# Kernel optimization log

Measured on AMD Instinct MI355X. Metric: run time of the kernel, lower is better.

The kernel has to match this reference:

```python
import jax, jax.numpy as jnp
import numpy as np

DIM = 256
N_STATE = 8
DT_RANK = 16  # ceil(dim/16)
D_CONV = 4
HIDDEN = 128  # dim * rank_ratio
EPS = 1e-6


def rmsnorm(x, w):
    # matches torch: x / (||x||_2 / sqrt(d) + eps) * w
    norm = jnp.sqrt(jnp.sum(x * x, axis=-1, keepdims=True))
    return x / (norm / np.sqrt(x.shape[-1]) + EPS) * w


def dwconv1d(x, w, b, pad_l, pad_r):
    # x: (b, l, c); w: (c, 1, k) depthwise
    out = jax.lax.conv_general_dilated(
        x.transpose(0, 2, 1), w, window_strides=(1,),
        padding=[(pad_l, pad_r)], dimension_numbers=('NCH', 'OIH', 'NCH'),
        feature_group_count=w.shape[0])
    return (out + b[None, :, None]).transpose(0, 2, 1)


def selective_scan(x, delta, A, Bm, Cm, D):
    # x, delta: (b,l,d); A: (d,n); Bm, Cm: (b,l,n); D: (d,)
    dA = jnp.exp(delta[..., None] * A)                     # (b,l,d,n)
    dBx = (delta * x)[..., None] * Bm[:, :, None, :]       # (b,l,d,n)

    def step(h, inp):
        dA_t, dBx_t, C_t = inp
        h = dA_t * h + dBx_t                               # (b,d,n)
        y = jnp.einsum('bdn,bn->bd', h, C_t)
        return h, y

    h0 = jnp.zeros((x.shape[0],) + A.shape, dtype=x.dtype)
    _, ys = jax.lax.scan(step, h0,
                         (dA.transpose(1, 0, 2, 3), dBx.transpose(1, 0, 2, 3),
                          Cm.transpose(1, 0, 2)))
    return ys.transpose(1, 0, 2) + x * D                   # (b,l,d)


def mamba_branch(x, ctx, conv_w, conv_b, xproj_w, dtproj_w, dtproj_b, A_log, D):
    xc = jax.nn.silu(dwconv1d(x, conv_w, conv_b, D_CONV - 1, 0))  # causal conv
    x_dbl = ctx @ xproj_w.T                                  # (b,l,r+2n)
    dt, Bm, Cm = jnp.split(x_dbl, [DT_RANK, DT_RANK + N_STATE], axis=-1)
    delta = jax.nn.softplus(dt @ dtproj_w.T + dtproj_b)
    A = -jnp.exp(A_log)
    return selective_scan(xc, delta, A, Bm, Cm, D)


def setup_inputs() -> dict:
    key = jax.random.key(0)
    ks = jax.random.split(key, 24)
    B, L, D = 4, 64 * 64, DIM
    s = 0.02
    A_log_init = jnp.log(jnp.broadcast_to(jnp.arange(1, N_STATE + 1, dtype=jnp.float32), (D, N_STATE)))
    dt_bias = jnp.full((D,), jnp.log(jnp.expm1(0.01)), dtype=jnp.float32)
    inp = {
        'x0': jax.random.normal(ks[0], (B, L, D), jnp.float32),
        'x1': jax.random.normal(ks[1], (B, L, D), jnp.float32),
        'w_norm0': jnp.ones((D,), jnp.float32),
        'w_norm1': jnp.ones((D,), jnp.float32),
        'in_proj_w': jax.random.normal(ks[2], (2 * D, D), jnp.float32) * s,
        'conv_w_f': jax.random.normal(ks[3], (D, 1, D_CONV), jnp.float32) * 0.3,
        'conv_b_f': jnp.zeros((D,), jnp.float32),
        'xproj_w_f': jax.random.normal(ks[4], (DT_RANK + 2 * N_STATE, D), jnp.float32) * s,
        'dtproj_w_f': jax.random.normal(ks[5], (D, DT_RANK), jnp.float32) * 0.1,
        'dtproj_b_f': dt_bias,
        'A_log_f': A_log_init,
        'D_f': jnp.ones((D,), jnp.float32),
        'conv_w_bw': jax.random.normal(ks[6], (D, 1, D_CONV), jnp.float32) * 0.3,
        'conv_b_bw': jnp.zeros((D,), jnp.float32),
        'xproj_w_bw': jax.random.normal(ks[7], (DT_RANK + 2 * N_STATE, D), jnp.float32) * s,
        'dtproj_w_bw': jax.random.normal(ks[8], (D, DT_RANK), jnp.float32) * 0.1,
        'dtproj_b_bw': dt_bias,
        'A_log_bw': A_log_init,
        'D_bw': jnp.ones((D,), jnp.float32),
        'norm_y_w': jnp.ones((D,), jnp.float32),
        'out_proj_w': jax.random.normal(ks[9], (D, D), jnp.float32) * s,
        'fc1_w': jax.random.normal(ks[10], (HIDDEN, D), jnp.float32) * s,
        'dw_w': jax.random.normal(ks[11], (HIDDEN, 1, 3), jnp.float32) * 0.3,
        'dw_b': jnp.zeros((HIDDEN,), jnp.float32),
        'fc2_w': jax.random.normal(ks[12], (D, HIDDEN), jnp.float32) * s,
    }
    return inp


def reference(x0, x1, w_norm0, w_norm1, in_proj_w, conv_w_f, conv_b_f, xproj_w_f,
              dtproj_w_f, dtproj_b_f, A_log_f, D_f, conv_w_bw, conv_b_bw,
              xproj_w_bw, dtproj_w_bw, dtproj_b_bw, A_log_bw, D_bw, norm_y_w,
              out_proj_w, fc1_w, dw_w, dw_b, fc2_w):
    residual = x0
    h0 = rmsnorm(x0, w_norm0)
    h1 = rmsnorm(x1, w_norm1)
    # cross-Mamba: main stream x0 -> x,z; extra_emb x1 -> dt/B/C
    xz = h0 @ in_proj_w.T
    xin, z = jnp.split(xz, 2, axis=-1)
    y_f = mamba_branch(xin, h1, conv_w_f, conv_b_f, xproj_w_f, dtproj_w_f,
                       dtproj_b_f, A_log_f, D_f)
    y_b = jnp.flip(mamba_branch(jnp.flip(xin, 1), jnp.flip(h1, 1), conv_w_bw,
                                conv_b_bw, xproj_w_bw, dtproj_w_bw, dtproj_b_bw,
                                A_log_bw, D_bw), 1)
    y = (y_f + y_b) * 0.5          # if_devide_out=True (bidirectional)
    y = rmsnorm(y, norm_y_w)       # use_norm=True
    y = y * jax.nn.silu(z)
    x = y @ out_proj_w.T + residual
    # LowRankFeedForward (dropout = identity at eval)
    m = x @ fc1_w.T
    m = jax.nn.silu(dwconv1d(m, dw_w, dw_b, 1, 1))
    m = m @ fc2_w.T
    return x + m
```

## Files before the change

kernel.cpp:

```cpp
#include <hip/hip_runtime.h>
#include <math.h>
#include <cstddef>

#define BB 4
#define LL 4096
#define DD 256
#define NST 8
#define RANK 16
#define HID 128
#define BL (BB*LL)
#define BLD ((size_t)BL*DD)
#define CH 256
#define CLEN 16
#define XZS 512

typedef __bf16 bf16x8 __attribute__((ext_vector_type(8)));
typedef float  f32x4  __attribute__((ext_vector_type(4)));

__device__ __forceinline__ float siluf(float x){ return x / (1.f + __expf(-x)); }
__device__ __forceinline__ float softplus_fast(float x){
  float r = __logf(1.f + __expf(x));
  return x > 15.f ? x : r;
}
__device__ __forceinline__ unsigned short f2bf(float x){
  union { float f; unsigned u; } v; v.f = x;
  unsigned r = v.u + 0x7fffu + ((v.u >> 16) & 1u);
  return (unsigned short)(r >> 16);
}
__device__ __forceinline__ float bf2f(unsigned short u){
  union { unsigned u32; float f; } c; c.u32 = ((unsigned)u) << 16;
  return c.f;
}

__global__ __launch_bounds__(64) void rms_kernel(
    const float* __restrict__ x0, const float* __restrict__ w0, unsigned short* __restrict__ o0b,
    const float* __restrict__ x1, const float* __restrict__ w1, unsigned short* __restrict__ o1b)
{
  const float* x; const float* w; unsigned short* o;
  if (blockIdx.y == 0){ x = x0; w = w0; o = o0b; } else { x = x1; w = w1; o = o1b; }
  size_t tok = blockIdx.x;
  int lane = threadIdx.x;
  float4 v = ((const float4*)(x + tok*DD))[lane];
  float s = v.x*v.x + v.y*v.y + v.z*v.z + v.w*v.w;
  #pragma unroll
  for (int m = 1; m < 64; m <<= 1) s += __shfl_xor(s, m, 64);
  float scale = 1.f / (sqrtf(s) * (1.f/16.f) + 1e-6f);
  float4 wv = ((const float4*)w)[lane];
  ushort4 r;
  r.x = f2bf(v.x*scale*wv.x); r.y = f2bf(v.y*scale*wv.y);
  r.z = f2bf(v.z*scale*wv.z); r.w = f2bf(v.w*scale*wv.w);
  ((ushort4*)(o + tok*DD))[lane] = r;
}

__global__ __launch_bounds__(256) void cvt_kernel(
    const float* __restrict__ sA,
    const float* __restrict__ s0, const float* __restrict__ s1,
    const float* __restrict__ s2, const float* __restrict__ s3,
    const float* __restrict__ s4,
    unsigned short* __restrict__ d1, unsigned short* __restrict__ d2)
{
  int i = blockIdx.x*256 + threadIdx.x;
  if (i >= 278528) return;
  if (i < 131072){ d1[i] = f2bf(sA[i]); return; }
  int j = i - 131072;
  float v;
  if (j < 8192)        v = s0[j];
  else if (j < 16384)  v = s1[j - 8192];
  else if (j < 81920)  v = s2[j - 16384];
  else if (j < 114688) v = s3[j - 81920];
  else                 v = s4[j - 114688];
  d2[j] = f2bf(v);
}

template<int EPI>
__global__ __launch_bounds__(256) void gemm_mfma(
    const unsigned short* __restrict__ A, const unsigned short* __restrict__ Bw,
    float* __restrict__ C, const float* __restrict__ Add,
    unsigned short* __restrict__ Cb, int M, int ldc, int K)
{
  constexpr int BK = 64, PAD = 8;
  __shared__ __align__(16) unsigned short As[64][BK+PAD];
  __shared__ __align__(16) unsigned short Bs[64][BK+PAD];
  int tid  = threadIdx.x;
  int row0 = blockIdx.x * 64;
  int col0 = blockIdx.y * 64;
  int wave = tid >> 6, lane = tid & 63;
  int wm = (wave >> 1) * 32, wn = (wave & 1) * 32;
  int lm = lane & 15, kq = lane >> 4;
  int sr = tid >> 2, sc16 = (tid & 3) * 16;

  f32x4 acc[2][2];
  #pragma unroll
  for (int i = 0; i < 2; i++)
    #pragma unroll
    for (int j = 0; j < 2; j++) acc[i][j] = (f32x4){0.f,0.f,0.f,0.f};

  for (int k0 = 0; k0 < K; k0 += BK){
    const unsigned short* ap = &A [(size_t)(row0 + sr)*K + k0 + sc16];
    const unsigned short* bp = &Bw[(size_t)(col0 + sr)*K + k0 + sc16];
    *(int4*)&As[sr][sc16]   = *(const int4*)ap;
    *(int4*)&As[sr][sc16+8] = *(const int4*)(ap + 8);
    *(int4*)&Bs[sr][sc16]   = *(const int4*)bp;
    *(int4*)&Bs[sr][sc16+8] = *(const int4*)(bp + 8);
    __syncthreads();
    #pragma unroll
    for (int ks = 0; ks < 2; ks++){
      bf16x8 af[2], bfv[2];
      #pragma unroll
      for (int i = 0; i < 2; i++) af[i]  = *(const bf16x8*)&As[wm + i*16 + lm][ks*32 + kq*8];
      #pragma unroll
      for (int j = 0; j < 2; j++) bfv[j] = *(const bf16x8*)&Bs[wn + j*16 + lm][ks*32 + kq*8];
      #pragma unroll
      for (int i = 0; i < 2; i++)
        #pragma unroll
        for (int j = 0; j < 2; j++)
          acc[i][j] = __builtin_amdgcn_mfma_f32_16x16x32_bf16(af[i], bfv[j], acc[i][j], 0, 0, 0);
    }
    __syncthreads();
  }

  #pragma unroll
  for (int i = 0; i < 2; i++){
    int rbase = row0 + wm + i*16 + kq*4;
    #pragma unroll
    for (int j = 0; j < 2; j++){
      int col = col0 + wn + j*16 + lm;
      #pragma unroll
      for (int r = 0; r < 4; r++){
        size_t idx = (size_t)(rbase + r)*ldc + col;
        float v = acc[i][j][r];
        if constexpr (EPI == 1 || EPI == 2) v += Add[idx];
        if constexpr (EPI != 3) C[idx] = v;
        if constexpr (EPI == 1 || EPI == 3) Cb[idx] = f2bf(v);
      }
    }
  }
}

__global__ __launch_bounds__(256) void front_kernel(
    const unsigned short* __restrict__ xz,
    const float* __restrict__ xd,
    const float* __restrict__ cwf, const float* __restrict__ cbf,
    const float* __restrict__ cwb, const float* __restrict__ cbb,
    const float* __restrict__ dtwf, const float* __restrict__ dtbf,
    const float* __restrict__ dtwb, const float* __restrict__ dtbb,
    const float* __restrict__ Alogf, const float* __restrict__ Alogb,
    const float* __restrict__ Dfp, const float* __restrict__ Dbp,
    unsigned int* __restrict__ xde,
    float* __restrict__ Sp, float* __restrict__ Hout)
{
  int chunk = blockIdx.x, b = blockIdx.y, dir = blockIdx.z;
  int s0 = chunk*CLEN;
  int d  = threadIdx.x;

  __shared__ float sdt[CLEN][16];
  __shared__ float sB [CLEN][8];
  __shared__ float sC [CLEN][8];
  #pragma unroll
  for (int e = threadIdx.x; e < CLEN*32; e += 256){
    int lt = e >> 5, col = e & 31;
    int pos = s0 + lt;
    int row = dir ? (LL-1-pos) : pos;
    float v = xd[((size_t)b*LL + row)*64 + dir*32 + col];
    if (col < 16)      sdt[lt][col]    = v;
    else if (col < 24) sB [lt][col-16] = v;
    else               sC [lt][col-24] = v;
  }
  __syncthreads();

  float4 cw = ((const float4*)(dir ? cwb : cwf))[d];
  float cb  = (dir ? cbb : cbf)[d];
  const float* dtw = (dir ? dtwb : dtwf) + d*RANK;
  float4 w0 = ((const float4*)dtw)[0], w1 = ((const float4*)dtw)[1];
  float4 w2 = ((const float4*)dtw)[2], w3 = ((const float4*)dtw)[3];
  float dtb = (dir ? dtbb : dtbf)[d];
  float Dd  = (dir ? Dbp : Dfp)[d];

  const unsigned short* xp = xz + (size_t)b*LL*XZS + d;
  #define LDX(pos) ((pos) >= 0 ? bf2f(xp[(size_t)(dir ? (LL-1-(pos)) : (pos))*XZS]) : 0.f)

  float xv[CLEN+3];
  xv[0] = LDX(s0-3); xv[1] = LDX(s0-2); xv[2] = LDX(s0-1);
  #pragma unroll
  for (int i = 0; i < CLEN; i++) xv[3+i] = LDX(s0+i);
  #undef LDX

  unsigned packX[CLEN];
  #pragma unroll
  for (int i = 0; i < CLEN; i++){
    float xc = cb;
    xc = fmaf(cw.x, xv[i],   xc); xc = fmaf(cw.y, xv[i+1], xc);
    xc = fmaf(cw.z, xv[i+2], xc); xc = fmaf(cw.w, xv[i+3], xc);
    xc = siluf(xc);
    const float* dt = &sdt[i][0];
    float de = dtb;
    de = fmaf(dt[0],w0.x, fmaf(dt[1],w0.y, fmaf(dt[2],w0.z, fmaf(dt[3],w0.w, de))));
    de = fmaf(dt[4],w1.x, fmaf(dt[5],w1.y, fmaf(dt[6],w1.z, fmaf(dt[7],w1.w, de))));
    de = fmaf(dt[8],w2.x, fmaf(dt[9],w2.y, fmaf(dt[10],w2.z, fmaf(dt[11],w2.w, de))));
    de = fmaf(dt[12],w3.x, fmaf(dt[13],w3.y, fmaf(dt[14],w3.z, fmaf(dt[15],w3.w, de))));
    de = softplus_fast(de);
    packX[i] = (unsigned)f2bf(xc) | ((unsigned)f2bf(de) << 16);
  }

  const float* Alog = dir ? Alogb : Alogf;
  float A[NST];
  bool fast = true;
  #pragma unroll
  for (int n = 0; n < NST; n++){
    A[n] = -__expf(Alog[d*NST + n]);
    fast = fast && (fabsf(A[n] + (float)(n+1)) < 1e-3f);
  }
  float h[NST];
  #pragma unroll
  for (int n = 0; n < NST; n++) h[n] = 0.f;
  float S = 0.f;

  unsigned int* xout = xde + ((size_t)(dir*BB + b)*LL + s0)*DD + d;

  if (fast){
    #pragma unroll
    for (int t = 0; t < CLEN; t++){
      unsigned pk = packX[t];
      float xc = bf2f((unsigned short)(pk & 0xffffu));
      float de = bf2f((unsigned short)(pk >> 16));
      S += de;
      float dux = de * xc;
      const float* Bv = &sB[t][0];
      const float* Cv = &sC[t][0];
      float e1 = __expf(-de);
      float dA = e1;
      float acc = xc * Dd;
      h[0] = fmaf(dA, h[0], dux*Bv[0]); acc = fmaf(h[0], Cv[0], acc); dA *= e1;
      h[1] = fmaf(dA, h[1], dux*Bv[1]); acc = fmaf(h[1], Cv[1], acc); dA *= e1;
      h[2] = fmaf(dA, h[2], dux*Bv[2]); acc = fmaf(h[2], Cv[2], acc); dA *= e1;
      h[3] = fmaf(dA, h[3], dux*Bv[3]); acc = fmaf(h[3], Cv[3], acc); dA *= e1;
      h[4] = fmaf(dA, h[4], dux*Bv[4]); acc = fmaf(h[4], Cv[4], acc); dA *= e1;
      h[5] = fmaf(dA, h[5], dux*Bv[5]); acc = fmaf(h[5], Cv[5], acc); dA *= e1;
      h[6] = fmaf(dA, h[6], dux*Bv[6]); acc = fmaf(h[6], Cv[6], acc); dA *= e1;
      h[7] = fmaf(dA, h[7], dux*Bv[7]); acc = fmaf(h[7], Cv[7], acc);
      xout[(size_t)t*DD] = (pk & 0xffff0000u) | (unsigned)f2bf(acc);
    }
  } else {
    #pragma unroll
    for (int t = 0; t < CLEN; t++){
      unsigned pk = packX[t];
      float xc = bf2f((unsigned short)(pk & 0xffffu));
      float de = bf2f((unsigned short)(pk >> 16));
      S += de;
      float dux = de * xc;
      const float* Bv = &sB[t][0];
      const float* Cv = &sC[t][0];
      float acc = xc * Dd;
      #pragma unroll
      for (int n = 0; n < NST; n++){
        h[n] = fmaf(__expf(de*A[n]), h[n], dux*Bv[n]);
        acc = fmaf(h[n], Cv[n], acc);
      }
      xout[(size_t)t*DD] = (pk & 0xffff0000u) | (unsigned)f2bf(acc);
    }
  }

  size_t ob = ((((size_t)dir*CH + chunk)*BB + b)*DD + d)*NST;
  float4 h0v, h1v;
  h0v.x=h[0]; h0v.y=h[1]; h0v.z=h[2]; h0v.w=h[3];
  h1v.x=h[4]; h1v.y=h[5]; h1v.z=h[6]; h1v.w=h[7];
  *(float4*)&Hout[ob]   = h0v; *(float4*)&Hout[ob+4] = h1v;
  Sp[((size_t)(dir*CH + chunk)*BB + b)*DD + d] = S;
}

__global__ __launch_bounds__(64) void scan_p2(
    const float* __restrict__ Sp, float* H,
    const float* __restrict__ Alogf, const float* __restrict__ Alogb)
{
  const int SEGC = CH/8;
  int blk = blockIdx.x;
  int d   = blk & (DD-1);
  int b   = (blk >> 8) & (BB-1);
  int dir = blk >> 10;
  int t   = threadIdx.x;
  int seg = t >> 3, n = t & 7;
  float A = -__expf((dir ? Alogb : Alogf)[d*NST + n]);

  const size_t sstr = (size_t)BB*DD;
  const size_t hstr = (size_t)BB*DD*NST;
  size_t sb = (size_t)dir*CH*sstr + (size_t)b*DD + d;
  size_t hb = (size_t)dir*CH*hstr + ((size_t)b*DD + d)*NST + n;
  int c0 = seg*SEGC;

  float pv[SEGC], hv[SEGC];
  #pragma unroll
  for (int k = 0; k < SEGC; k++){
    pv[k] = Sp[sb + (size_t)(c0+k)*sstr];
    hv[k] = H [hb + (size_t)(c0+k)*hstr];
  }
  float h = 0.f, Ss = 0.f;
  #pragma unroll
  for (int k = 0; k < SEGC; k++){
    Ss += pv[k];
    pv[k] = __expf(pv[k]*A);
    h = fmaf(pv[k], h, hv[k]);
  }
  float pi = __expf(Ss*A), hi = h;
  #pragma unroll
  for (int off = 8; off < 64; off <<= 1){
    float hprev = __shfl_up(hi, off, 64);
    float pprev = __shfl_up(pi, off, 64);
    if (t >= off){ hi = fmaf(pi, hprev, hi); pi *= pprev; }
  }
  float hin = __shfl_up(hi, 8, 64);
  h = (seg == 0) ? 0.f : hin;
  #pragma unroll
  for (int k = 0; k < SEGC; k++){
    size_t idx = hb + (size_t)(c0+k)*hstr;
    H[idx] = h;
    h = fmaf(pv[k], h, hv[k]);
  }
}

__global__ __launch_bounds__(256) void back_kernel(
    const unsigned int* __restrict__ xde,
    const float* __restrict__ xd,
    const float* __restrict__ Alogf, const float* __restrict__ Alogb,
    const float* __restrict__ Hin,
    const unsigned short* __restrict__ xz,
    const float* __restrict__ wn,
    unsigned short* __restrict__ outb)
{
  int c  = blockIdx.x, b = blockIdx.y;
  int cbk = CH-1-c;
  int d  = threadIdx.x;
  int T0 = c*CLEN;
  int Pb = cbk*CLEN;

  __shared__ float sCf[CLEN][8], sCb[CLEN][8];
  __shared__ float red[CLEN][4];
  __shared__ float sscale[CLEN];
  {
    int k  = threadIdx.x & 7;
    int lt = (threadIdx.x >> 3) & 15;
    if (threadIdx.x < 128)
      sCf[lt][k] = xd[((size_t)b*LL + T0 + lt)*64 + 24 + k];
    else
      sCb[lt][k] = xd[((size_t)b*LL + (T0 + 15 - lt))*64 + 56 + k];
  }
  __syncthreads();

  float Af[NST], Ab[NST];
  bool fast = true;
  #pragma unroll
  for (int n = 0; n < NST; n++){
    Af[n] = -__expf(Alogf[d*NST + n]);
    Ab[n] = -__expf(Alogb[d*NST + n]);
    fast = fast && (fabsf(Af[n] + (float)(n+1)) < 1e-3f)
                && (fabsf(Ab[n] + (float)(n+1)) < 1e-3f);
  }

  float vf[CLEN];

  {
    float hn[NST];
    size_t ib = (((size_t)c*BB + b)*DD + d)*NST;
    float4 a0 = *(const float4*)&Hin[ib];
    float4 a1 = *(const float4*)&Hin[ib+4];
    hn[0]=a0.x; hn[1]=a0.y; hn[2]=a0.z; hn[3]=a0.w;
    hn[4]=a1.x; hn[5]=a1.y; hn[6]=a1.z; hn[7]=a1.w;
    const unsigned int* p = xde + ((size_t)b*LL + T0)*DD + d;
    unsigned int pk[CLEN];
    #pragma unroll
    for (int t = 0; t < CLEN; t++) pk[t] = p[(size_t)t*DD];
    float S = 0.f;
    if (fast){
      #pragma unroll
      for (int t = 0; t < CLEN; t++){
        float y0 = bf2f((unsigned short)(pk[t] & 0xffffu));
        float de = bf2f((unsigned short)(pk[t] >> 16));
        S += de;
        float E = __expf(-S);
        float q = E;
        float corr = q * (hn[0]*sCf[t][0]);
        q *= E; corr = fmaf(q, hn[1]*sCf[t][1], corr);
        q *= E; corr = fmaf(q, hn[2]*sCf[t][2], corr);
        q *= E; corr = fmaf(q, hn[3]*sCf[t][3], corr);
        q *= E; corr = fmaf(q, hn[4]*sCf[t][4], corr);
        q *= E; corr = fmaf(q, hn[5]*sCf[t][5], corr);
        q *= E; corr = fmaf(q, hn[6]*sCf[t][6], corr);
        q *= E; corr = fmaf(q, hn[7]*sCf[t][7], corr);
        vf[t] = y0 + corr;
      }
    } else {
      #pragma unroll
      for (int t = 0; t < CLEN; t++){
        float y0 = bf2f((unsigned short)(pk[t] & 0xffffu));
        float de = bf2f((unsigned short)(pk[t] >> 16));
        S += de;
        float corr = 0.f;
        #pragma unroll
        for (int n = 0; n < NST; n++)
          corr = fmaf(__expf(S*Af[n]), hn[n]*sCf[t][n], corr);
        vf[t] = y0 + corr;
      }
    }
  }

  {
    float hn[NST];
    size_t ib = ((((size_t)CH + cbk)*BB + b)*DD + d)*NST;
    float4 a0 = *(const float4*)&Hin[ib];
    float4 a1 = *(const float4*)&Hin[ib+4];
    hn[0]=a0.x; hn[1]=a0.y; hn[2]=a0.z; hn[3]=a0.w;
    hn[4]=a1.x; hn[5]=a1.y; hn[6]=a1.z; hn[7]=a1.w;
    const unsigned int* p = xde + ((size_t)(BB + b)*LL + Pb)*DD + d;
    unsigned int pk[CLEN];
    #pragma unroll
    for (int t = 0; t < CLEN; t++) pk[t] = p[(size_t)t*DD];
    float S = 0.f;
    if (fast){
      #pragma unroll
      for (int t = 0; t < CLEN; t++){
        float y0 = bf2f((unsigned short)(pk[t] & 0xffffu));
        float de = bf2f((unsigned short)(pk[t] >> 16));
        S += de;
        float E = __expf(-S);
        float q = E;
        float corr = q * (hn[0]*sCb[t][0]);
        q *= E; corr = fmaf(q, hn[1]*sCb[t][1], corr);
        q *= E; corr = fmaf(q, hn[2]*sCb[t][2], corr);
        q *= E; corr = fmaf(q, hn[3]*sCb[t][3], corr);
        q *= E; corr = fmaf(q, hn[4]*sCb[t][4], corr);
        q *= E; corr = fmaf(q, hn[5]*sCb[t][5], corr);
        q *= E; corr = fmaf(q, hn[6]*sCb[t][6], corr);
        q *= E; corr = fmaf(q, hn[7]*sCb[t][7], corr);
        int j = 15 - t;
        vf[j] = 0.5f*(vf[j] + y0 + corr);
      }
    } else {
      #pragma unroll
      for (int t = 0; t < CLEN; t++){
        float y0 = bf2f((unsigned short)(pk[t] & 0xffffu));
        float de = bf2f((unsigned short)(pk[t] >> 16));
        S += de;
        float corr = 0.f;
        #pragma unroll
        for (int n = 0; n < NST; n++)
          corr = fmaf(__expf(S*Ab[n]), hn[n]*sCb[t][n], corr);
        int j = 15 - t;
        vf[j] = 0.5f*(vf[j] + y0 + corr);
      }
    }
  }

  int wave = d >> 6, lane = d & 63;
  #pragma unroll
  for (int j = 0; j < CLEN; j++){
    float s = vf[j]*vf[j];
    #pragma unroll
    for (int m = 1; m < 64; m <<= 1) s += __shfl_xor(s, m, 64);
    if (lane == 0) red[j][wave] = s;
  }
  __syncthreads();
  if (d < CLEN){
    float s = red[d][0] + red[d][1] + red[d][2] + red[d][3];
    sscale[d] = 1.f / (sqrtf(s)*(1.f/16.f) + 1e-6f);
  }
  __syncthreads();

  float wd = wn[d];
  #pragma unroll
  for (int j = 0; j < CLEN; j++){
    size_t tok = (size_t)b*LL + T0 + j;
    float z = bf2f(xz[tok*XZS + 256 + d]);
    outb[tok*DD + d] = f2bf(vf[j]*sscale[j]*wd*siluf(z));
  }
}

__global__ __launch_bounds__(256) void dwconv3_kernel(
    const float* __restrict__ m, const float* __restrict__ w,
    const float* __restrict__ bi, unsigned short* __restrict__ o)
{
  size_t gid = (size_t)blockIdx.x*256 + threadIdx.x;
  int c4  = (int)(gid & 31) * 4;
  int tok = (int)(gid >> 5);
  int b = tok >> 12, t = tok & (LL-1);
  float4 acc = {bi[c4], bi[c4+1], bi[c4+2], bi[c4+3]};
  #pragma unroll
  for (int k = 0; k < 3; k++){
    int tt = t - 1 + k;
    if (tt >= 0 && tt < LL){
      float4 mv = *(const float4*)&m[((size_t)b*LL + tt)*HID + c4];
      acc.x = fmaf(w[c4*3 + k],       mv.x, acc.x);
      acc.y = fmaf(w[(c4+1)*3 + k],   mv.y, acc.y);
      acc.z = fmaf(w[(c4+2)*3 + k],   mv.z, acc.z);
      acc.w = fmaf(w[(c4+3)*3 + k],   mv.w, acc.w);
    }
  }
  ushort4 r;
  r.x = f2bf(siluf(acc.x)); r.y = f2bf(siluf(acc.y));
  r.z = f2bf(siluf(acc.z)); r.w = f2bf(siluf(acc.w));
  *(ushort4*)&o[gid*4] = r;
}

extern "C" void kernel_launch(void* const* d_in, const int* in_sizes, int n_in,
                              void* d_out, int out_size, void* d_ws, size_t ws_size,
                              hipStream_t stream)
{
  const float* x0        = (const float*)d_in[0];
  const float* x1        = (const float*)d_in[1];
  const float* w_norm0   = (const float*)d_in[2];
  const float* w_norm1   = (const float*)d_in[3];
  const float* in_proj_w = (const float*)d_in[4];
  const float* conv_w_f  = (const float*)d_in[5];
  const float* conv_b_f  = (const float*)d_in[6];
  const float* xproj_w_f = (const float*)d_in[7];
  const float* dtproj_w_f= (const float*)d_in[8];
  const float* dtproj_b_f= (const float*)d_in[9];
  const float* A_log_f   = (const float*)d_in[10];
  const float* D_f       = (const float*)d_in[11];
  const float* conv_w_bw = (const float*)d_in[12];
  const float* conv_b_bw = (const float*)d_in[13];
  const float* xproj_w_bw= (const float*)d_in[14];
  const float* dtproj_w_bw=(const float*)d_in[15];
  const float* dtproj_b_bw=(const float*)d_in[16];
  const float* A_log_bw  = (const float*)d_in[17];
  const float* D_bw      = (const float*)d_in[18];
  const float* norm_y_w  = (const float*)d_in[19];
  const float* out_proj_w= (const float*)d_in[20];
  const float* fc1_w     = (const float*)d_in[21];
  const float* dw_w      = (const float*)d_in[22];
  const float* dw_b      = (const float*)d_in[23];
  const float* fc2_w     = (const float*)d_in[24];
  float* out = (float*)d_out;
  float* ws  = (float*)d_ws;

  float* r0 = ws + 0*BLD;
  float* r1 = ws + 1*BLD;
  float* r2 = ws + 2*BLD;
  float* r3 = ws + 3*BLD;
  float* r4 = ws + 4*BLD;
  float* r5 = ws + 5*BLD;
  float* r6 = ws + 6*BLD;
  float* r7 = ws + 7*BLD;

  unsigned short* h0b   = (unsigned short*)r0;
  unsigned short* h1b   = (unsigned short*)r1;
  unsigned short* xz_b  = (unsigned short*)r2;
  float*          xd    = r3;
  unsigned int*   xde   = (unsigned int*)r4;
  unsigned short* wbuf1 = (unsigned short*)r6;
  float* Hout = r6;
  float* Hin  = Hout;
  const size_t SPLANE = (size_t)2*CH*BB*DD;
  float* Sp   = r7 + (BLD - SPLANE);
  unsigned short* ycomb_b = (unsigned short*)r0;
  unsigned short* wbuf2   = (unsigned short*)r7;
  unsigned short* wb_xp   = wbuf2;
  unsigned short* wb_out  = wbuf2 + 16384;
  unsigned short* wb_fc1  = wbuf2 + 81920;
  unsigned short* wb_fc2  = wbuf2 + 114688;
  unsigned short* xb      = wbuf2 + 147456;
  float*          m1      = r4;
  unsigned short* m2b     = (unsigned short*)r5;

  cvt_kernel<<<dim3(1088), 256, 0, stream>>>(
      in_proj_w, xproj_w_f, xproj_w_bw, out_proj_w, fc1_w, fc2_w, wbuf1, wbuf2);

  rms_kernel<<<dim3(BL,2), 64, 0, stream>>>(x0, w_norm0, h0b, x1, w_norm1, h1b);

  gemm_mfma<3><<<dim3(BL/64, 8), 256, 0, stream>>>(
      h0b, wbuf1, nullptr, nullptr, xz_b, BL, XZS, 256);

  gemm_mfma<0><<<dim3(BL/64, 1), 256, 0, stream>>>(
      h1b, wb_xp, xd, nullptr, nullptr, BL, 64, 256);

  front_kernel<<<dim3(CH, BB, 2), 256, 0, stream>>>(
      xz_b, xd, conv_w_f, conv_b_f, conv_w_bw, conv_b_bw,
      dtproj_w_f, dtproj_b_f, dtproj_w_bw, dtproj_b_bw,
      A_log_f, A_log_bw, D_f, D_bw, xde, Sp, Hout);

  scan_p2<<<dim3(2*BB*DD), 64, 0, stream>>>(Sp, Hout, A_log_f, A_log_bw);

  back_kernel<<<dim3(CH, BB), 256, 0, stream>>>(
      xde, xd, A_log_f, A_log_bw, Hin, xz_b, norm_y_w, ycomb_b);

  gemm_mfma<1><<<dim3(BL/64, 4), 256, 0, stream>>>(
      ycomb_b, wb_out, out, x0, xb, BL, 256, 256);

  gemm_mfma<0><<<dim3(BL/64, 2), 256, 0, stream>>>(
      xb, wb_fc1, m1, nullptr, nullptr, BL, 128, 256);

  dwconv3_kernel<<<dim3((BL*HID/4)/256), 256, 0, stream>>>(m1, dw_w, dw_b, m2b);

  gemm_mfma<2><<<dim3(BL/64, 4), 256, 0, stream>>>(
      m2b, wb_fc2, out, out, nullptr, BL, 256, 128);
}
```

Before: 261.0 us.

## Fuse preprocessing, projection GEMMs, and depthwise conv into fewer kernels

Merges rmsnorm and weight conversion into one launch, and runs the in_proj and x_proj GEMMs in a single grid. The bf16 copy of the residual output is dropped: fc1 now reads the fp32 output and converts it while staging its tiles. The depthwise conv plus SiLU is computed inside the fc2 GEMM's A-tile load, so the standalone dwconv kernel and the m2b buffer go away. This cuts launch count and intermediate traffic, but fc2 now re-reads three neighbouring rows of m1 for each column tile.

```diff
diff --git a/kernel.cpp b/kernel.cpp
--- a/kernel.cpp
+++ b/kernel.cpp
@@ -32,34 +32,34 @@
   return c.f;
 }
 
-__global__ __launch_bounds__(64) void rms_kernel(
+__global__ __launch_bounds__(256) void pre_kernel(
     const float* __restrict__ x0, const float* __restrict__ w0, unsigned short* __restrict__ o0b,
-    const float* __restrict__ x1, const float* __restrict__ w1, unsigned short* __restrict__ o1b)
-{
-  const float* x; const float* w; unsigned short* o;
-  if (blockIdx.y == 0){ x = x0; w = w0; o = o0b; } else { x = x1; w = w1; o = o1b; }
-  size_t tok = blockIdx.x;
-  int lane = threadIdx.x;
-  float4 v = ((const float4*)(x + tok*DD))[lane];
-  float s = v.x*v.x + v.y*v.y + v.z*v.z + v.w*v.w;
-  #pragma unroll
-  for (int m = 1; m < 64; m <<= 1) s += __shfl_xor(s, m, 64);
-  float scale = 1.f / (sqrtf(s) * (1.f/16.f) + 1e-6f);
-  float4 wv = ((const float4*)w)[lane];
-  ushort4 r;
-  r.x = f2bf(v.x*scale*wv.x); r.y = f2bf(v.y*scale*wv.y);
-  r.z = f2bf(v.z*scale*wv.z); r.w = f2bf(v.w*scale*wv.w);
-  ((ushort4*)(o + tok*DD))[lane] = r;
-}
-
-__global__ __launch_bounds__(256) void cvt_kernel(
+    const float* __restrict__ x1, const float* __restrict__ w1, unsigned short* __restrict__ o1b,
     const float* __restrict__ sA,
     const float* __restrict__ s0, const float* __restrict__ s1,
     const float* __restrict__ s2, const float* __restrict__ s3,
     const float* __restrict__ s4,
     unsigned short* __restrict__ d1, unsigned short* __restrict__ d2)
 {
-  int i = blockIdx.x*256 + threadIdx.x;
+  int blk = blockIdx.x;
+  if (blk < 8192){
+    const float* x; const float* w; unsigned short* o; size_t tok;
+    int wv = threadIdx.x >> 6, lane = threadIdx.x & 63;
+    if (blk < 4096){ x = x0; w = w0; o = o0b; tok = (size_t)blk*4 + wv; }
+    else           { x = x1; w = w1; o = o1b; tok = (size_t)(blk-4096)*4 + wv; }
+    float4 v = ((const float4*)(x + tok*DD))[lane];
+    float s = v.x*v.x + v.y*v.y + v.z*v.z + v.w*v.w;
+    #pragma unroll
+    for (int m = 1; m < 64; m <<= 1) s += __shfl_xor(s, m, 64);
+    float scale = 1.f / (sqrtf(s) * (1.f/16.f) + 1e-6f);
+    float4 wvv = ((const float4*)w)[lane];
+    ushort4 r;
+    r.x = f2bf(v.x*scale*wvv.x); r.y = f2bf(v.y*scale*wvv.y);
+    r.z = f2bf(v.z*scale*wvv.z); r.w = f2bf(v.w*scale*wvv.w);
+    ((ushort4*)(o + tok*DD))[lane] = r;
+    return;
+  }
+  int i = (blk - 8192)*256 + threadIdx.x;
   if (i >= 278528) return;
   if (i < 131072){ d1[i] = f2bf(sA[i]); return; }
   int j = i - 131072;
@@ -129,9 +129,224 @@
       for (int r = 0; r < 4; r++){
         size_t idx = (size_t)(rbase + r)*ldc + col;
         float v = acc[i][j][r];
-        if constexpr (EPI == 1 || EPI == 2) v += Add[idx];
+        if constexpr (EPI == 2) v += Add[idx];
         if constexpr (EPI != 3) C[idx] = v;
-        if constexpr (EPI == 1 || EPI == 3) Cb[idx] = f2bf(v);
+        if constexpr (EPI == 3) Cb[idx] = f2bf(v);
+      }
+    }
+  }
+}
+
+__global__ __launch_bounds__(256) void gemm_xzxp(
+    const unsigned short* __restrict__ A0, const unsigned short* __restrict__ A1,
+    const unsigned short* __restrict__ B0, const unsigned short* __restrict__ B1,
+    unsigned short* __restrict__ Cxz, float* __restrict__ Cxd)
+{
+  constexpr int BK = 64, PAD = 8, K = 256;
+  __shared__ __align__(16) unsigned short As[64][BK+PAD];
+  __shared__ __align__(16) unsigned short Bs[64][BK+PAD];
+  int tid  = threadIdx.x;
+  bool xp  = (blockIdx.y == 8);
+  const unsigned short* A  = xp ? A1 : A0;
+  const unsigned short* Bw = xp ? B1 : B0;
+  int row0 = blockIdx.x * 64;
+  int col0 = xp ? 0 : blockIdx.y * 64;
+  int wave = tid >> 6, lane = tid & 63;
+  int wm = (wave >> 1) * 32, wn = (wave & 1) * 32;
+  int lm = lane & 15, kq = lane >> 4;
+  int sr = tid >> 2, sc16 = (tid & 3) * 16;
+
+  f32x4 acc[2][2];
+  #pragma unroll
+  for (int i = 0; i < 2; i++)
+    #pragma unroll
+    for (int j = 0; j < 2; j++) acc[i][j] = (f32x4){0.f,0.f,0.f,0.f};
+
+  for (int k0 = 0; k0 < K; k0 += BK){
+    const unsigned short* ap = &A [(size_t)(row0 + sr)*K + k0 + sc16];
+    const unsigned short* bp = &Bw[(size_t)(col0 + sr)*K + k0 + sc16];
+    *(int4*)&As[sr][sc16]   = *(const int4*)ap;
+    *(int4*)&As[sr][sc16+8] = *(const int4*)(ap + 8);
+    *(int4*)&Bs[sr][sc16]   = *(const int4*)bp;
+    *(int4*)&Bs[sr][sc16+8] = *(const int4*)(bp + 8);
+    __syncthreads();
+    #pragma unroll
+    for (int ks = 0; ks < 2; ks++){
+      bf16x8 af[2], bfv[2];
+      #pragma unroll
+      for (int i = 0; i < 2; i++) af[i]  = *(const bf16x8*)&As[wm + i*16 + lm][ks*32 + kq*8];
+      #pragma unroll
+      for (int j = 0; j < 2; j++) bfv[j] = *(const bf16x8*)&Bs[wn + j*16 + lm][ks*32 + kq*8];
+      #pragma unroll
+      for (int i = 0; i < 2; i++)
+        #pragma unroll
+        for (int j = 0; j < 2; j++)
+          acc[i][j] = __builtin_amdgcn_mfma_f32_16x16x32_bf16(af[i], bfv[j], acc[i][j], 0, 0, 0);
+    }
+    __syncthreads();
+  }
+
+  #pragma unroll
+  for (int i = 0; i < 2; i++){
+    int rbase = row0 + wm + i*16 + kq*4;
+    #pragma unroll
+    for (int j = 0; j < 2; j++){
+      int col = col0 + wn + j*16 + lm;
+      #pragma unroll
+      for (int r = 0; r < 4; r++){
+        float v = acc[i][j][r];
+        if (xp) Cxd[(size_t)(rbase + r)*64  + col] = v;
+        else    Cxz[(size_t)(rbase + r)*XZS + col] = f2bf(v);
+      }
+    }
+  }
+}
+
+__global__ __launch_bounds__(256) void gemm_fc1(
+    const float* __restrict__ A, const unsigned short* __restrict__ Bw,
+    float* __restrict__ C)
+{
+  constexpr int BK = 64, PAD = 8, K = 256, LDC = 128;
+  __shared__ __align__(16) unsigned short As[64][BK+PAD];
+  __shared__ __align__(16) unsigned short Bs[64][BK+PAD];
+  int tid  = threadIdx.x;
+  int row0 = blockIdx.x * 64;
+  int col0 = blockIdx.y * 64;
+  int wave = tid >> 6, lane = tid & 63;
+  int wm = (wave >> 1) * 32, wn = (wave & 1) * 32;
+  int lm = lane & 15, kq = lane >> 4;
+  int sr = tid >> 2, sc16 = (tid & 3) * 16;
+
+  f32x4 acc[2][2];
+  #pragma unroll
+  for (int i = 0; i < 2; i++)
+    #pragma unroll
+    for (int j = 0; j < 2; j++) acc[i][j] = (f32x4){0.f,0.f,0.f,0.f};
+
+  for (int k0 = 0; k0 < K; k0 += BK){
+    const float* ap = &A[(size_t)(row0 + sr)*K + k0 + sc16];
+    #pragma unroll
+    for (int q = 0; q < 4; q++){
+      float4 f = *(const float4*)(ap + q*4);
+      ushort4 u; u.x = f2bf(f.x); u.y = f2bf(f.y); u.z = f2bf(f.z); u.w = f2bf(f.w);
+      *(ushort4*)&As[sr][sc16 + q*4] = u;
+    }
+    const unsigned short* bp = &Bw[(size_t)(col0 + sr)*K + k0 + sc16];
+    *(int4*)&Bs[sr][sc16]   = *(const int4*)bp;
+    *(int4*)&Bs[sr][sc16+8] = *(const int4*)(bp + 8);
+    __syncthreads();
+    #pragma unroll
+    for (int ks = 0; ks < 2; ks++){
+      bf16x8 af[2], bfv[2];
+      #pragma unroll
+      for (int i = 0; i < 2; i++) af[i]  = *(const bf16x8*)&As[wm + i*16 + lm][ks*32 + kq*8];
+      #pragma unroll
+      for (int j = 0; j < 2; j++) bfv[j] = *(const bf16x8*)&Bs[wn + j*16 + lm][ks*32 + kq*8];
+      #pragma unroll
+      for (int i = 0; i < 2; i++)
+        #pragma unroll
+        for (int j = 0; j < 2; j++)
+          acc[i][j] = __builtin_amdgcn_mfma_f32_16x16x32_bf16(af[i], bfv[j], acc[i][j], 0, 0, 0);
+    }
+    __syncthreads();
+  }
+
+  #pragma unroll
+  for (int i = 0; i < 2; i++){
+    int rbase = row0 + wm + i*16 + kq*4;
+    #pragma unroll
+    for (int j = 0; j < 2; j++){
+      int col = col0 + wn + j*16 + lm;
+      #pragma unroll
+      for (int r = 0; r < 4; r++)
+        C[(size_t)(rbase + r)*LDC + col] = acc[i][j][r];
+    }
+  }
+}
+
+__global__ __launch_bounds__(256) void gemm_fc2dw(
+    const float* __restrict__ m1, const unsigned short* __restrict__ Bw,
+    const float* __restrict__ dww, const float* __restrict__ dwb,
+    float* __restrict__ C)
+{
+  constexpr int BK = 64, PAD = 8, K = 128, LDC = 256;
+  __shared__ __align__(16) unsigned short As[64][BK+PAD];
+  __shared__ __align__(16) unsigned short Bs[64][BK+PAD];
+  __shared__ float wS[HID*3];
+  __shared__ float bS[HID];
+  int tid  = threadIdx.x;
+  if (tid < HID){
+    bS[tid] = dwb[tid];
+    wS[tid*3+0] = dww[tid*3+0];
+    wS[tid*3+1] = dww[tid*3+1];
+    wS[tid*3+2] = dww[tid*3+2];
+  }
+  __syncthreads();
+
+  int row0 = blockIdx.x * 64;
+  int col0 = blockIdx.y * 64;
+  int wave = tid >> 6, lane = tid & 63;
+  int wm = (wave >> 1) * 32, wn = (wave & 1) * 32;
+  int lm = lane & 15, kq = lane >> 4;
+  int sr = tid >> 2, sc16 = (tid & 3) * 16;
+  int r16 = tid >> 4, cc = (tid & 15) * 4;
+
+  f32x4 acc[2][2];
+  #pragma unroll
+  for (int i = 0; i < 2; i++)
+    #pragma unroll
+    for (int j = 0; j < 2; j++) acc[i][j] = (f32x4){0.f,0.f,0.f,0.f};
+
+  for (int k0 = 0; k0 < K; k0 += BK){
+    #pragma unroll
+    for (int pp = 0; pp < 4; pp++){
+      int r = pp*16 + r16;
+      int t = row0 + r;
+      int tl = t & (LL-1);
+      int c = k0 + cc;
+      const float* mrow = &m1[(size_t)t*HID + c];
+      float4 vm = *(const float4*)mrow;
+      float4 vp = (tl > 0)      ? *(const float4*)(mrow - HID) : (float4){0,0,0,0};
+      float4 vn = (tl < LL-1)   ? *(const float4*)(mrow + HID) : (float4){0,0,0,0};
+      float a0 = bS[c+0] + wS[(c+0)*3]*vp.x + wS[(c+0)*3+1]*vm.x + wS[(c+0)*3+2]*vn.x;
+      float a1 = bS[c+1] + wS[(c+1)*3]*vp.y + wS[(c+1)*3+1]*vm.y + wS[(c+1)*3+2]*vn.y;
+      float a2 = bS[c+2] + wS[(c+2)*3]*vp.z + wS[(c+2)*3+1]*vm.z + wS[(c+2)*3+2]*vn.z;
+      float a3 = bS[c+3] + wS[(c+3)*3]*vp.w + wS[(c+3)*3+1]*vm.w + wS[(c+3)*3+2]*vn.w;
+      ushort4 u;
+      u.x = f2bf(siluf(a0)); u.y = f2bf(siluf(a1));
+      u.z = f2bf(siluf(a2)); u.w = f2bf(siluf(a3));
+      *(ushort4*)&As[r][cc] = u;
+    }
+    const unsigned short* bp = &Bw[(size_t)(col0 + sr)*K + k0 + sc16];
+    *(int4*)&Bs[sr][sc16]   = *(const int4*)bp;
+    *(int4*)&Bs[sr][sc16+8] = *(const int4*)(bp + 8);
+    __syncthreads();
+    #pragma unroll
+    for (int ks = 0; ks < 2; ks++){
+      bf16x8 af[2], bfv[2];
+      #pragma unroll
+      for (int i = 0; i < 2; i++) af[i]  = *(const bf16x8*)&As[wm + i*16 + lm][ks*32 + kq*8];
+      #pragma unroll
+      for (int j = 0; j < 2; j++) bfv[j] = *(const bf16x8*)&Bs[wn + j*16 + lm][ks*32 + kq*8];
+      #pragma unroll
+      for (int i = 0; i < 2; i++)
+        #pragma unroll
+        for (int j = 0; j < 2; j++)
+          acc[i][j] = __builtin_amdgcn_mfma_f32_16x16x32_bf16(af[i], bfv[j], acc[i][j], 0, 0, 0);
+    }
+    __syncthreads();
+  }
+
+  #pragma unroll
+  for (int i = 0; i < 2; i++){
+    int rbase = row0 + wm + i*16 + kq*4;
+    #pragma unroll
+    for (int j = 0; j < 2; j++){
+      int col = col0 + wn + j*16 + lm;
+      #pragma unroll
+      for (int r = 0; r < 4; r++){
+        size_t idx = (size_t)(rbase + r)*LDC + col;
+        C[idx] = C[idx] + acc[i][j][r];
       }
     }
   }
@@ -471,32 +686,6 @@
     float z = bf2f(xz[tok*XZS + 256 + d]);
     outb[tok*DD + d] = f2bf(vf[j]*sscale[j]*wd*siluf(z));
   }
-}
-
-__global__ __launch_bounds__(256) void dwconv3_kernel(
-    const float* __restrict__ m, const float* __restrict__ w,
-    const float* __restrict__ bi, unsigned short* __restrict__ o)
-{
-  size_t gid = (size_t)blockIdx.x*256 + threadIdx.x;
-  int c4  = (int)(gid & 31) * 4;
-  int tok = (int)(gid >> 5);
-  int b = tok >> 12, t = tok & (LL-1);
-  float4 acc = {bi[c4], bi[c4+1], bi[c4+2], bi[c4+3]};
-  #pragma unroll
-  for (int k = 0; k < 3; k++){
-    int tt = t - 1 + k;
-    if (tt >= 0 && tt < LL){
-      float4 mv = *(const float4*)&m[((size_t)b*LL + tt)*HID + c4];
-      acc.x = fmaf(w[c4*3 + k],       mv.x, acc.x);
-      acc.y = fmaf(w[(c4+1)*3 + k],   mv.y, acc.y);
-      acc.z = fmaf(w[(c4+2)*3 + k],   mv.z, acc.z);
-      acc.w = fmaf(w[(c4+3)*3 + k],   mv.w, acc.w);
-    }
-  }
-  ushort4 r;
-  r.x = f2bf(siluf(acc.x)); r.y = f2bf(siluf(acc.y));
-  r.z = f2bf(siluf(acc.z)); r.w = f2bf(siluf(acc.w));
-  *(ushort4*)&o[gid*4] = r;
 }
 
 extern "C" void kernel_launch(void* const* d_in, const int* in_sizes, int n_in,
@@ -556,20 +745,14 @@
   unsigned short* wb_out  = wbuf2 + 16384;
   unsigned short* wb_fc1  = wbuf2 + 81920;
   unsigned short* wb_fc2  = wbuf2 + 114688;
-  unsigned short* xb      = wbuf2 + 147456;
   float*          m1      = r4;
-  unsigned short* m2b     = (unsigned short*)r5;
-
-  cvt_kernel<<<dim3(1088), 256, 0, stream>>>(
+
+  pre_kernel<<<dim3(9280), 256, 0, stream>>>(
+      x0, w_norm0, h0b, x1, w_norm1, h1b,
       in_proj_w, xproj_w_f, xproj_w_bw, out_proj_w, fc1_w, fc2_w, wbuf1, wbuf2);
 
-  rms_kernel<<<dim3(BL,2), 64, 0, stream>>>(x0, w_norm0, h0b, x1, w_norm1, h1b);
-
-  gemm_mfma<3><<<dim3(BL/64, 8), 256, 0, stream>>>(
-      h0b, wbuf1, nullptr, nullptr, xz_b, BL, XZS, 256);
-
-  gemm_mfma<0><<<dim3(BL/64, 1), 256, 0, stream>>>(
-      h1b, wb_xp, xd, nullptr, nullptr, BL, 64, 256);
+  gemm_xzxp<<<dim3(BL/64, 9), 256, 0, stream>>>(
+      h0b, h1b, wbuf1, wb_xp, xz_b, xd);
 
   front_kernel<<<dim3(CH, BB, 2), 256, 0, stream>>>(
       xz_b, xd, conv_w_f, conv_b_f, conv_w_bw, conv_b_bw,
@@ -581,14 +764,10 @@
   back_kernel<<<dim3(CH, BB), 256, 0, stream>>>(
       xde, xd, A_log_f, A_log_bw, Hin, xz_b, norm_y_w, ycomb_b);
 
-  gemm_mfma<1><<<dim3(BL/64, 4), 256, 0, stream>>>(
-      ycomb_b, wb_out, out, x0, xb, BL, 256, 256);
-
-  gemm_mfma<0><<<dim3(BL/64, 2), 256, 0, stream>>>(
-      xb, wb_fc1, m1, nullptr, nullptr, BL, 128, 256);
-
-  dwconv3_kernel<<<dim3((BL*HID/4)/256), 256, 0, stream>>>(m1, dw_w, dw_b, m2b);
-
   gemm_mfma<2><<<dim3(BL/64, 4), 256, 0, stream>>>(
-      m2b, wb_fc2, out, out, nullptr, BL, 256, 128);
-}
+      ycomb_b, wb_out, out, x0, nullptr, BL, 256, 256);
+
+  gemm_fc1<<<dim3(BL/64, 2), 256, 0, stream>>>(out, wb_fc1, m1);
+
+  gemm_fc2dw<<<dim3(BL/64, 4), 256, 0, stream>>>(m1, wb_fc2, dw_w, dw_b, out);
+}
```

Measured after the change: 251.8 us. -3.5%, faster.
